# Optimization experiments

Measured on AMD Instinct MI355X. Metric: run time of the kernel, lower is better.

The kernel has to match this reference:

```python
import jax, jax.numpy as jnp
import numpy as np

NUM_CLASSES = 128
COST_CLS = 2.0
COST_BBOX = 0.25
ALPHA = 0.25
GAMMA = 2.0
BBOX_NORM = np.array([1.0, 1.0, 1.0, 0.1, 0.1, 0.1, 1.0, 1.0, 0.1, 0.1], dtype=np.float32)


def _lsa(cost):
    # Jonker-Volgenant style shortest augmenting path Hungarian (e-maxx formulation).
    # cost: (n, m) float64 with n <= m. Returns col4row: for each row i, assigned column.
    n, m = cost.shape
    INF = 1e18
    a = np.zeros((n + 1, m + 1))
    a[1:, 1:] = cost
    u = np.zeros(n + 1)
    v = np.zeros(m + 1)
    p = np.zeros(m + 1, dtype=np.int64)   # p[j]: row (1-indexed) assigned to col j
    way = np.zeros(m + 1, dtype=np.int64)
    cols = np.arange(1, m + 1)
    for i in range(1, n + 1):
        p[0] = i
        j0 = 0
        minv = np.full(m + 1, INF)
        used = np.zeros(m + 1, dtype=bool)
        while True:
            used[j0] = True
            i0 = p[j0]
            cur = a[i0, 1:] - u[i0] - v[1:]
            better = (~used[1:]) & (cur < minv[1:])
            jb = cols[better]
            minv[jb] = cur[better]
            way[jb] = j0
            free = cols[~used[1:]]
            j1 = free[np.argmin(minv[free])]
            delta = minv[j1]
            uj = np.flatnonzero(used)
            u[p[uj]] += delta
            v[uj] -= delta
            nj = np.flatnonzero(~used)
            minv[nj] -= delta
            j0 = int(j1)
            if p[j0] == 0:
                break
        while j0:
            j1 = way[j0]
            p[j0] = p[j1]
            j0 = j1
    col4row = np.zeros(n, dtype=np.int64)
    for j in range(1, m + 1):
        if p[j]:
            col4row[p[j] - 1] = j - 1
    return col4row


def _match(cls_scores, bbox_preds, gt_labels, gt_bboxes):
    # Matching is done under no_grad in the original; host-side numpy mirrors scipy lsa.
    cs = np.asarray(cls_scores, np.float64)
    bp = np.asarray(bbox_preds, np.float64)
    gl = np.asarray(gt_labels)
    gb = np.asarray(gt_bboxes, np.float64)
    B = cs.shape[0]
    norm = BBOX_NORM.astype(np.float64)
    pred_idx = np.zeros(gl.shape, dtype=np.int64)
    for b in range(B):
        prob = 1.0 / (1.0 + np.exp(-np.clip(cs[b], -20.0, 20.0)))
        cost_cls = -prob[:, gl[b]]                                   # (Q, G)
        pn = np.clip(bp[b] / norm, -100, 100)
        gn = np.clip(gb[b] / norm, -100, 100)
        cost_bbox = np.abs(pn[:, None, :] - gn[None, :, :]).sum(-1)  # (Q, G) L1 cdist
        C = COST_CLS * cost_cls + COST_BBOX * cost_bbox
        pred_idx[b] = _lsa(C.T)   # for each gt g, its matched query index
    return pred_idx


def setup_inputs() -> dict:
    key = jax.random.key(0)
    k1, k2, k3, k4 = jax.random.split(key, 4)
    B, Q, G, C = 64, 2048, 64, NUM_CLASSES
    return {
        "cls_scores": jax.random.normal(k1, (B, Q, C), jnp.float32),
        "bbox_preds": jax.random.normal(k2, (B, Q, 10), jnp.float32),
        "gt_labels": jax.random.randint(k3, (B, G), 0, C),
        "gt_bboxes": jax.random.normal(k4, (B, G, 10), jnp.float32),
    }


def reference(cls_scores, bbox_preds, gt_labels, gt_bboxes):
    pred_idx = jnp.asarray(_match(cls_scores, bbox_preds, gt_labels, gt_bboxes))  # [B, G]
    B, Q, C = cls_scores.shape
    G = gt_labels.shape[1]
    b_idx = jnp.arange(B)[:, None]
    # one-hot classification targets at matched (query, label) positions
    onehot = jnp.zeros((B, Q, C), cls_scores.dtype).at[b_idx, pred_idx, gt_labels].set(1.0)
    prob = jax.nn.sigmoid(cls_scores)
    ce = -(onehot * jax.nn.log_sigmoid(cls_scores)
           + (1.0 - onehot) * jax.nn.log_sigmoid(-cls_scores))
    p_t = prob * onehot + (1.0 - prob) * (1.0 - onehot)
    focal_w = (ALPHA * onehot + (1.0 - ALPHA) * (1.0 - onehot)) * (1.0 - p_t) ** GAMMA
    loss_cls = (ce * focal_w).sum() / (G * B)   # per-batch sum / num_gt, then mean over B
    norm = jnp.asarray(BBOX_NORM)
    mp = bbox_preds[b_idx, pred_idx]            # [B, G, 10] matched predictions
    mg = gt_bboxes                              # gt_indices == arange(G): every gt matched
    loss_bbox = jnp.abs(mp / norm - mg / norm).mean()
    ml = cls_scores[b_idx, pred_idx]
    pos_acc = (jnp.argmax(ml, -1) == gt_labels).astype(jnp.float32).mean()
    xyz_err = jnp.abs(mp[..., :3] - mg[..., :3]).mean()
    matched = jnp.float32(G)
    return jnp.stack([loss_cls, loss_bbox, matched, pos_acc, xyz_err])
```

## Files before the change

### kernel.cpp

```cpp
#include <hip/hip_runtime.h>
#include <hip/hip_fp16.h>
#include <math.h>

#define NB 64
#define NQ 2048
#define NG 64
#define NC 128
#define TPB 256

#define WS_NEG   0
#define WS_POS   16384
#define WS_PRED  147456
#define WS_COST  163840
#define WS_NEED  (163840 + (size_t)NB * NG * NQ * 2)

__device__ __forceinline__ float normd(int d) {
    return (d == 3 || d == 4 || d == 5 || d == 8 || d == 9) ? 0.1f : 1.0f;
}
__device__ __forceinline__ float softplus_f(float x) {
    return x > 0.f ? x + log1pf(expf(-x)) : log1pf(expf(x));
}
__device__ __forceinline__ double neg_term(float x) {
    float s = 1.f / (1.f + expf(-x));
    return (double)(0.75f * s * s * softplus_f(x));
}
__device__ __forceinline__ double pos_term(float x) {
    float s = 1.f / (1.f + expf(-x));
    float om = 1.f - s;
    return (double)(0.25f * om * om * softplus_f(-x));
}
__device__ __forceinline__ float neg_term_fast(float x) {
    const float m = fmaxf(x, 0.f);
    const float a = __expf(x - m);
    const float bq = __expf(-m);
    const float den = a + bq;
    const float s = __fdividef(a, den);
    const float sp = m + __logf(den);
    return 0.75f * s * s * sp;
}

__device__ __forceinline__ unsigned dpp_min6(unsigned key) {
    unsigned t;
    t = (unsigned)__builtin_amdgcn_update_dpp((int)key, (int)key, 0x111, 0xF, 0xF, false);
    key = t < key ? t : key;
    t = (unsigned)__builtin_amdgcn_update_dpp((int)key, (int)key, 0x112, 0xF, 0xF, false);
    key = t < key ? t : key;
    t = (unsigned)__builtin_amdgcn_update_dpp((int)key, (int)key, 0x114, 0xF, 0xF, false);
    key = t < key ? t : key;
    t = (unsigned)__builtin_amdgcn_update_dpp((int)key, (int)key, 0x118, 0xF, 0xF, false);
    key = t < key ? t : key;
    t = (unsigned)__builtin_amdgcn_update_dpp((int)key, (int)key, 0x142, 0xF, 0xF, false);
    key = t < key ? t : key;
    t = (unsigned)__builtin_amdgcn_update_dpp((int)key, (int)key, 0x143, 0xF, 0xF, false);
    key = t < key ? t : key;
    return key;
}

__global__ __launch_bounds__(TPB) void cost_neg_kernel(
    const float* __restrict__ cls, const float* __restrict__ bp,
    const int* __restrict__ gl, const float* __restrict__ gb,
    unsigned short* __restrict__ Ch, double* __restrict__ negP)
{
    const int b = blockIdx.x >> 5;
    const int q0 = (blockIdx.x & 31) << 6;
    const int tid = threadIdx.x;
    __shared__ float cls_s[64 * 129];
    __shared__ float pn_s[10 * 64];
    __shared__ float gn_s[64 * 10];
    __shared__ int lbl_s[64];

    double negsum = 0.0;
    const float* clsb = cls + ((size_t)b * NQ + q0) * NC;
    const float4* cls4 = reinterpret_cast<const float4*>(clsb);
    #pragma unroll
    for (int it = 0; it < 8; ++it) {
        const int idx4 = it * TPB + tid;
        const float4 xv = cls4[idx4];
        const int e0 = idx4 << 2;
        float* dst = &cls_s[(e0 >> 7) * 129 + (e0 & 127)];
        dst[0] = xv.x; dst[1] = xv.y; dst[2] = xv.z; dst[3] = xv.w;
        const float s4 = neg_term_fast(xv.x) + neg_term_fast(xv.y)
                       + neg_term_fast(xv.z) + neg_term_fast(xv.w);
        negsum += (double)s4;
    }
    const float* bpb = bp + ((size_t)b * NQ + q0) * 10;
    for (int idx = tid; idx < 640; idx += TPB) {
        const int q = idx / 10, d = idx % 10;
        const float val = bpb[idx] / normd(d);
        pn_s[d * 64 + q] = fminf(100.f, fmaxf(-100.f, val));
    }
    const float* gbb = gb + (size_t)b * NG * 10;
    for (int idx = tid; idx < 640; idx += TPB) {
        const int g = idx / 10, d = idx % 10;
        const float val = gbb[idx] / normd(d);
        gn_s[g * 10 + d] = fminf(100.f, fmaxf(-100.f, val));
    }
    if (tid < NG) lbl_s[tid] = gl[b * NG + tid];
    __syncthreads();

    const int q = tid & 63;
    float pnq[10];
    #pragma unroll
    for (int d = 0; d < 10; ++d) pnq[d] = pn_s[d * 64 + q];
    for (int g = tid >> 6; g < NG; g += 4) {
        const int lbl = lbl_s[g];
        float x = cls_s[q * 129 + lbl];
        x = fminf(20.f, fmaxf(-20.f, x));
        const float s = __fdividef(1.f, 1.f + __expf(-x));
        float cb = 0.f;
        #pragma unroll
        for (int d = 0; d < 10; ++d) cb += fabsf(pnq[d] - gn_s[g * 10 + d]);
        const float cost = -2.f * s + 0.25f * cb;
        Ch[((size_t)(b * NG + g)) * NQ + q0 + q] =
            __builtin_bit_cast(unsigned short, __float2half_rn(cost));
    }

    #pragma unroll
    for (int off = 32; off; off >>= 1) negsum += __shfl_down(negsum, off);
    __shared__ double bsum[4];
    if ((tid & 63) == 0) bsum[tid >> 6] = negsum;
    __syncthreads();
    if (tid == 0) negP[blockIdx.x] = bsum[0] + bsum[1] + bsum[2] + bsum[3];
}

__device__ __forceinline__ void jv_row(
    const int i, uint4 (&buf)[4], const unsigned short* __restrict__ Cb16,
    float (&vv)[32], unsigned& amask, const int lane, const int qbase,
    float* u, float* usedD, int* p, int* way32)
{
    float cf[32];
    #pragma unroll
    for (int m = 0; m < 4; ++m) {
        const unsigned arr[4] = {buf[m].x, buf[m].y, buf[m].z, buf[m].w};
        #pragma unroll
        for (int d = 0; d < 4; ++d) {
            const __half2 h = __builtin_bit_cast(__half2, arr[d]);
            cf[m * 8 + d * 2]     = __low2float(h);
            cf[m * 8 + d * 2 + 1] = __high2float(h);
        }
    }
    float madj[32];
    unsigned m0 = 0xFFFFFFFFu, m1 = 0xFFFFFFFFu, m2 = 0xFFFFFFFFu, m3 = 0xFFFFFFFFu;
    #pragma unroll
    for (int k = 0; k < 32; ++k) {
        const float cand = cf[k] - vv[k];
        madj[k] = cand;
        const unsigned kb = (__float_as_uint(cand) & 0xFFFFF800u) | (unsigned)(qbase + k);
        if ((k & 3) == 0)      m0 = kb < m0 ? kb : m0;
        else if ((k & 3) == 1) m1 = kb < m1 ? kb : m1;
        else if ((k & 3) == 2) m2 = kb < m2 ? kb : m2;
        else                   m3 = kb < m3 ? kb : m3;
    }
    if (i + 2 <= NG) {
        const uint4* rp = reinterpret_cast<const uint4*>(
                              Cb16 + (size_t)(i + 1) * NQ) + lane * 4;
        buf[0] = rp[0]; buf[1] = rp[1]; buf[2] = rp[2]; buf[3] = rp[3];
    }
    const unsigned ma = m0 < m1 ? m0 : m1;
    const unsigned mb = m2 < m3 ? m2 : m3;
    unsigned gkey = (unsigned)__builtin_amdgcn_readlane(
                        (int)dpp_min6(ma < mb ? ma : mb), 63);
    int q1 = (int)(gkey & 2047u);
    float D = __uint_as_float(gkey & 0xFFFFF800u);
    int ow = q1 >> 5, kk = q1 & 31;
    unsigned am_ow = (unsigned)__builtin_amdgcn_readlane((int)amask, ow);

    if (!((am_ow >> kk) & 1u)) {
        if (lane == 0) { u[i] += D; p[q1 + 1] = i; }
    } else {
        unsigned um = 0;
        if (lane == ow) { um |= 1u << kk; usedD[q1 + 1] = D; }
        #pragma unroll
        for (int k = 0; k < 32; ++k)
            if (k == kk && lane == ow) madj[k] = 1e30f;
        int j0 = q1 + 1;
        int i0 = p[j0];
        while (true) {
            const float s = u[i0] - D;
            const uint4* rp = reinterpret_cast<const uint4*>(
                                  Cb16 + (size_t)(i0 - 1) * NQ) + lane * 4;
            const uint4 t[4] = {rp[0], rp[1], rp[2], rp[3]};
            float tc[32];
            #pragma unroll
            for (int m = 0; m < 4; ++m) {
                const unsigned arr[4] = {t[m].x, t[m].y, t[m].z, t[m].w};
                #pragma unroll
                for (int d = 0; d < 4; ++d) {
                    const __half2 h = __builtin_bit_cast(__half2, arr[d]);
                    tc[m * 8 + d * 2]     = __low2float(h);
                    tc[m * 8 + d * 2 + 1] = __high2float(h);
                }
            }
            unsigned bk = 0xFFFFFFFFu;
            #pragma unroll
            for (int k = 0; k < 32; ++k) {
                const float cand = tc[k] - vv[k] - s;
                if (!((um >> k) & 1u) && cand < madj[k]) {
                    madj[k] = cand;
                    way32[qbase + k + 1] = (i << 16) | j0;
                }
                const unsigned kb = (__float_as_uint(madj[k]) & 0xFFFFF800u)
                                  | (unsigned)(qbase + k);
                bk = kb < bk ? kb : bk;
            }
            gkey = (unsigned)__builtin_amdgcn_readlane((int)dpp_min6(bk), 63);
            q1 = (int)(gkey & 2047u);
            D = __uint_as_float(gkey & 0xFFFFF800u);
            ow = q1 >> 5; kk = q1 & 31;
            am_ow = (unsigned)__builtin_amdgcn_readlane((int)amask, ow);
            if (!((am_ow >> kk) & 1u)) break;
            if (lane == ow) { um |= 1u << kk; usedD[q1 + 1] = D; }
            #pragma unroll
            for (int k = 0; k < 32; ++k)
                if (k == kk && lane == ow) madj[k] = 1e30f;
            j0 = q1 + 1;
            i0 = p[j0];
        }
        #pragma unroll
        for (int k = 0; k < 32; ++k) {
            if ((um >> k) & 1u) {
                const int j = qbase + k + 1;
                const float dd = D - usedD[j];
                vv[k] -= dd;
                u[p[j]] += dd;
            }
        }
        if (lane == 0) {
            u[i] += D;
            int j = q1 + 1;
            while (true) {
                const int w = way32[j];
                const int par = ((w >> 16) == i) ? (w & 0xFFFF) : 0;
                p[j] = par ? p[par] : i;
                if (!par) break;
                j = par;
            }
        }
    }
    if (lane == ow) amask |= 1u << kk;
}

__global__ __launch_bounds__(64, 1) void hungarian6_kernel(
    const unsigned short* __restrict__ Ch, int* __restrict__ pred)
{
    const int b = blockIdx.x;
    const int lane = threadIdx.x;
    __shared__ float u[NG + 1];
    __shared__ float usedD[NQ + 1];
    __shared__ int p[NQ + 1];
    __shared__ int way32[NQ + 1];

    for (int j = lane; j <= NQ; j += 64) { p[j] = 0; way32[j] = 0; }
    if (lane <= NG) u[lane] = 0.f;
    __syncthreads();

    const unsigned short* Cb16 = Ch + (size_t)b * NG * NQ;
    const int qbase = lane << 5;

    float vv[32];
    #pragma unroll
    for (int k = 0; k < 32; ++k) vv[k] = -16.f;
    unsigned amask = 0;

    uint4 A[4], B[4];
    {
        const uint4* r0 = reinterpret_cast<const uint4*>(Cb16) + lane * 4;
        const uint4* r1 = reinterpret_cast<const uint4*>(Cb16 + NQ) + lane * 4;
        A[0] = r0[0]; A[1] = r0[1]; A[2] = r0[2]; A[3] = r0[3];
        B[0] = r1[0]; B[1] = r1[1]; B[2] = r1[2]; B[3] = r1[3];
    }

    for (int i = 1; i <= NG; i += 2) {
        jv_row(i,     A, Cb16, vv, amask, lane, qbase, u, usedD, p, way32);
        jv_row(i + 1, B, Cb16, vv, amask, lane, qbase, u, usedD, p, way32);
    }

    for (int j = lane + 1; j <= NQ; j += 64) {
        const int pi = p[j];
        if (pi > 0) pred[b * NG + pi - 1] = j - 1;
    }
}

__global__ __launch_bounds__(TPB) void hungarian_fb_kernel(
    const float* __restrict__ cls, const float* __restrict__ bp,
    const int* __restrict__ gl, const float* __restrict__ gb,
    int* __restrict__ pred)
{
    const int b = blockIdx.x;
    const int tid = threadIdx.x;
    __shared__ float pn[10][NQ];
    __shared__ float gn[NG][10];
    __shared__ int lbls[NG];
    __shared__ double u[NG + 1];
    __shared__ double v[NQ + 1];
    __shared__ double minv[NQ + 1];
    __shared__ int p[NQ + 1];
    __shared__ int way[NQ + 1];
    __shared__ unsigned char used[NQ + 4];
    __shared__ double red_v[4];
    __shared__ int red_j[4];
    __shared__ int s_j0;
    __shared__ double s_delta;

    const float* bpb = bp + (size_t)b * NQ * 10;
    for (int idx = tid; idx < NQ * 10; idx += TPB) {
        int q = idx / 10, d = idx % 10;
        float val = bpb[idx] / normd(d);
        pn[d][q] = fminf(100.f, fmaxf(-100.f, val));
    }
    const float* gbb = gb + (size_t)b * NG * 10;
    for (int idx = tid; idx < NG * 10; idx += TPB) {
        int g = idx / 10, d = idx % 10;
        float val = gbb[idx] / normd(d);
        gn[g][d] = fminf(100.f, fmaxf(-100.f, val));
    }
    if (tid < NG) lbls[tid] = gl[b * NG + tid];
    for (int j = tid; j <= NQ; j += TPB) { v[j] = 0.0; p[j] = 0; way[j] = 0; }
    if (tid <= NG) u[tid] = 0.0;
    __syncthreads();

    const float* clsb = cls + (size_t)b * NQ * NC;

    for (int i = 1; i <= NG; ++i) {
        for (int j = tid; j <= NQ; j += TPB) { minv[j] = 1e18; used[j] = 0; }
        if (tid == 0) { p[0] = i; s_j0 = 0; }
        __syncthreads();
        while (true) {
            const int j0 = s_j0;
            if (tid == 0) used[j0] = 1;
            __syncthreads();
            const int i0 = p[j0];
            const int g = i0 - 1;
            const int lbl = lbls[g];
            const double ui0 = u[i0];
            double bestv = 1e30; int bestj = NQ + 1;
            for (int j = tid + 1; j <= NQ; j += TPB) {
                if (!used[j]) {
                    const int q = j - 1;
                    float x = clsb[(size_t)q * NC + lbl];
                    x = fminf(20.f, fmaxf(-20.f, x));
                    const double prob = 1.0 / (1.0 + exp((double)(-x)));
                    float cb = 0.f;
                    #pragma unroll
                    for (int d = 0; d < 10; ++d) cb += fabsf(pn[d][q] - gn[g][d]);
                    const double cur = -2.0 * prob + 0.25 * (double)cb - ui0 - v[j];
                    if (cur < minv[j]) { minv[j] = cur; way[j] = j0; }
                    const double mv = minv[j];
                    if (mv < bestv) { bestv = mv; bestj = j; }
                }
            }
            #pragma unroll
            for (int off = 32; off; off >>= 1) {
                const double ov = __shfl_down(bestv, off);
                const int oj = __shfl_down(bestj, off);
                if (ov < bestv || (ov == bestv && oj < bestj)) { bestv = ov; bestj = oj; }
            }
            if ((tid & 63) == 0) { red_v[tid >> 6] = bestv; red_j[tid >> 6] = bestj; }
            __syncthreads();
            if (tid == 0) {
                for (int w = 1; w < 4; ++w)
                    if (red_v[w] < bestv || (red_v[w] == bestv && red_j[w] < bestj)) {
                        bestv = red_v[w]; bestj = red_j[w];
                    }
                s_delta = bestv; s_j0 = bestj;
            }
            __syncthreads();
            const double delta = s_delta;
            const int j1 = s_j0;
            for (int j = tid; j <= NQ; j += TPB) {
                if (used[j]) { u[p[j]] += delta; v[j] -= delta; }
                else minv[j] -= delta;
            }
            __syncthreads();
            if (p[j1] == 0) break;
        }
        if (tid == 0) {
            int j = s_j0;
            while (j) { const int jn = way[j]; p[j] = p[jn]; j = jn; }
        }
        __syncthreads();
    }

    for (int j = tid + 1; j <= NQ; j += TPB) {
        const int pi = p[j];
        if (pi > 0) pred[b * NG + pi - 1] = j - 1;
    }
}

__global__ __launch_bounds__(TPB) void neg_fb_kernel(const float* __restrict__ cls,
                                                     double* __restrict__ negP, long n4) {
    const long stride = (long)gridDim.x * blockDim.x;
    double sum = 0.0;
    for (long i = (long)blockIdx.x * blockDim.x + threadIdx.x; i < n4; i += stride) {
        const float4 xv = reinterpret_cast<const float4*>(cls)[i];
        sum += (double)neg_term_fast(xv.x) + (double)neg_term_fast(xv.y)
             + (double)neg_term_fast(xv.z) + (double)neg_term_fast(xv.w);
    }
    #pragma unroll
    for (int off = 32; off; off >>= 1) sum += __shfl_down(sum, off);
    __shared__ double bsum[4];
    if ((threadIdx.x & 63) == 0) bsum[threadIdx.x >> 6] = sum;
    __syncthreads();
    if (threadIdx.x == 0) negP[blockIdx.x] = bsum[0] + bsum[1] + bsum[2] + bsum[3];
}

__global__ __launch_bounds__(TPB) void pos_kernel(
    const float* __restrict__ cls, const float* __restrict__ bp,
    const int* __restrict__ gl, const float* __restrict__ gb,
    const int* __restrict__ pred, double* __restrict__ posP)
{
    const int wid = (int)((blockIdx.x * blockDim.x + threadIdx.x) >> 6);
    const int lane = threadIdx.x & 63;
    if (wid >= NB * NG) return;
    const int b = wid >> 6;
    const int pq = pred[wid];
    const int lbl = gl[wid];
    const float* row = cls + ((size_t)b * NQ + pq) * NC;
    const float v1 = row[lane];
    const float v2 = row[lane + 64];
    float bv; int bi;
    if (v2 > v1) { bv = v2; bi = lane + 64; } else { bv = v1; bi = lane; }
    #pragma unroll
    for (int off = 32; off; off >>= 1) {
        const float ov = __shfl_down(bv, off);
        const int oi = __shfl_down(bi, off);
        if (ov > bv || (ov == bv && oi < bi)) { bv = ov; bi = oi; }
    }
    const float xl = __shfl(v1, lbl & 63);
    const float xh = __shfl(v2, lbl & 63);
    const float x = (lbl < 64) ? xl : xh;
    double bterm = 0.0, xterm = 0.0;
    if (lane < 10) {
        const float mp = bp[((size_t)b * NQ + pq) * 10 + lane];
        const float mg = gb[(size_t)wid * 10 + lane];
        const float nr = normd(lane);
        bterm = (double)fabsf(mp / nr - mg / nr);
        if (lane < 3) xterm = (double)fabsf(mp - mg);
    }
    #pragma unroll
    for (int off = 8; off; off >>= 1) {
        bterm += __shfl_down(bterm, off);
        xterm += __shfl_down(xterm, off);
    }
    if (lane == 0) {
        double* e = posP + (size_t)wid * 4;
        e[0] = pos_term(x) - neg_term(x);
        e[1] = bterm;
        e[2] = (bi == lbl) ? 1.0 : 0.0;
        e[3] = xterm;
    }
}

__global__ __launch_bounds__(TPB) void final_kernel(const double* __restrict__ ws,
                                                    float* __restrict__ out) {
    const int tid = threadIdx.x;
    const double* negP = ws;
    const double* posP = ws + 2048;
    double s[5] = {0, 0, 0, 0, 0};
    for (int i = tid; i < 2048; i += TPB) s[0] += negP[i];
    for (int i = tid; i < 4096; i += TPB) {
        const double* e = posP + (size_t)i * 4;
        s[1] += e[0]; s[2] += e[1]; s[3] += e[2]; s[4] += e[3];
    }
    __shared__ double red[4][5];
    #pragma unroll
    for (int c = 0; c < 5; ++c) {
        #pragma unroll
        for (int off = 32; off; off >>= 1) s[c] += __shfl_down(s[c], off);
    }
    if ((tid & 63) == 0) {
        #pragma unroll
        for (int c = 0; c < 5; ++c) red[tid >> 6][c] = s[c];
    }
    __syncthreads();
    if (tid == 0) {
        #pragma unroll
        for (int c = 0; c < 5; ++c) s[c] = red[0][c] + red[1][c] + red[2][c] + red[3][c];
        out[0] = (float)((s[0] + s[1]) / 4096.0);
        out[1] = (float)(s[2] / 40960.0);
        out[2] = 64.0f;
        out[3] = (float)(s[3] / 4096.0);
        out[4] = (float)(s[4] / 12288.0);
    }
}

extern "C" void kernel_launch(void* const* d_in, const int* in_sizes, int n_in,
                              void* d_out, int out_size, void* d_ws, size_t ws_size,
                              hipStream_t stream) {
    const float* cls = (const float*)d_in[0];
    const float* bp  = (const float*)d_in[1];
    const int*   gl  = (const int*)d_in[2];
    const float* gb  = (const float*)d_in[3];
    float* out = (float*)d_out;
    double* negP = (double*)((char*)d_ws + WS_NEG);
    double* posP = (double*)((char*)d_ws + WS_POS);
    int* pred    = (int*)((char*)d_ws + WS_PRED);
    unsigned short* Ch = (unsigned short*)((char*)d_ws + WS_COST);

    if (ws_size >= WS_NEED) {
        hipLaunchKernelGGL(cost_neg_kernel, dim3(NB * 32), dim3(TPB), 0, stream,
                           cls, bp, gl, gb, Ch, negP);
        hipLaunchKernelGGL(hungarian6_kernel, dim3(NB), dim3(64), 0, stream, Ch, pred);
    } else {
        hipLaunchKernelGGL(hungarian_fb_kernel, dim3(NB), dim3(TPB), 0, stream,
                           cls, bp, gl, gb, pred);
        const long n4 = (long)NB * NQ * NC / 4;
        hipLaunchKernelGGL(neg_fb_kernel, dim3(2048), dim3(TPB), 0, stream, cls, negP, n4);
    }
    hipLaunchKernelGGL(pos_kernel, dim3((NB * NG * 64) / TPB), dim3(TPB), 0, stream,
                       cls, bp, gl, gb, pred, posP);
    hipLaunchKernelGGL(final_kernel, dim3(1), dim3(TPB), 0, stream, (double*)d_ws, out);
}
```

Baseline: 189.3 us.

## Keep row duals in registers, deepen row prefetch, simplify focal term

The Hungarian kernel now holds the row dual u in a per-lane register instead of shared memory. It reads the value with readlane inside the augmenting search and applies dual updates through a small shared scratch array. Row prefetch goes from two buffered rows to four, and the first-pass min reduction is fused into the half-to-float conversion. The focal negative term uses a cheaper sigmoid/softplus form without the max-shift, which risks overflow for large positive logits, and the extra row buffers raise register pressure.

```diff
diff --git a/kernel.cpp b/kernel.cpp
--- a/kernel.cpp
+++ b/kernel.cpp
@@ -30,12 +30,10 @@
     return (double)(0.25f * om * om * softplus_f(-x));
 }
 __device__ __forceinline__ float neg_term_fast(float x) {
-    const float m = fmaxf(x, 0.f);
-    const float a = __expf(x - m);
-    const float bq = __expf(-m);
-    const float den = a + bq;
-    const float s = __fdividef(a, den);
-    const float sp = m + __logf(den);
+    const float t = __expf(x);
+    const float opt = 1.f + t;
+    const float s = t * __frcp_rn(opt);
+    const float sp = __logf(opt);
     return 0.75f * s * s * sp;
 }
 
@@ -55,6 +53,10 @@
     key = t < key ? t : key;
     return key;
 }
+__device__ __forceinline__ float readlane_f(float v, int lane) {
+    return __uint_as_float((unsigned)__builtin_amdgcn_readlane(
+               (int)__float_as_uint(v), lane));
+}
 
 __global__ __launch_bounds__(TPB) void cost_neg_kernel(
     const float* __restrict__ cls, const float* __restrict__ bp,
@@ -125,35 +127,30 @@
 
 __device__ __forceinline__ void jv_row(
     const int i, uint4 (&buf)[4], const unsigned short* __restrict__ Cb16,
-    float (&vv)[32], unsigned& amask, const int lane, const int qbase,
-    float* u, float* usedD, int* p, int* way32)
+    float (&vv)[32], unsigned& amask, float& u_reg, const int lane,
+    const int qbase, float* usedD, int* p, int* way32, float* uscr)
 {
-    float cf[32];
+    float madj[32];
+    unsigned m0 = 0xFFFFFFFFu, m1 = 0xFFFFFFFFu, m2 = 0xFFFFFFFFu, m3 = 0xFFFFFFFFu;
     #pragma unroll
     for (int m = 0; m < 4; ++m) {
         const unsigned arr[4] = {buf[m].x, buf[m].y, buf[m].z, buf[m].w};
         #pragma unroll
         for (int d = 0; d < 4; ++d) {
             const __half2 h = __builtin_bit_cast(__half2, arr[d]);
-            cf[m * 8 + d * 2]     = __low2float(h);
-            cf[m * 8 + d * 2 + 1] = __high2float(h);
+            const int k0 = m * 8 + d * 2;
+            const float c0 = __low2float(h) - vv[k0];
+            const float c1 = __high2float(h) - vv[k0 + 1];
+            madj[k0] = c0; madj[k0 + 1] = c1;
+            const unsigned kb0 = (__float_as_uint(c0) & 0xFFFFF800u) | (unsigned)(qbase + k0);
+            const unsigned kb1 = (__float_as_uint(c1) & 0xFFFFF800u) | (unsigned)(qbase + k0 + 1);
+            if (d & 1) { m2 = kb0 < m2 ? kb0 : m2;  m3 = kb1 < m3 ? kb1 : m3; }
+            else       { m0 = kb0 < m0 ? kb0 : m0;  m1 = kb1 < m1 ? kb1 : m1; }
         }
     }
-    float madj[32];
-    unsigned m0 = 0xFFFFFFFFu, m1 = 0xFFFFFFFFu, m2 = 0xFFFFFFFFu, m3 = 0xFFFFFFFFu;
-    #pragma unroll
-    for (int k = 0; k < 32; ++k) {
-        const float cand = cf[k] - vv[k];
-        madj[k] = cand;
-        const unsigned kb = (__float_as_uint(cand) & 0xFFFFF800u) | (unsigned)(qbase + k);
-        if ((k & 3) == 0)      m0 = kb < m0 ? kb : m0;
-        else if ((k & 3) == 1) m1 = kb < m1 ? kb : m1;
-        else if ((k & 3) == 2) m2 = kb < m2 ? kb : m2;
-        else                   m3 = kb < m3 ? kb : m3;
-    }
-    if (i + 2 <= NG) {
+    if (i + 4 <= NG) {
         const uint4* rp = reinterpret_cast<const uint4*>(
-                              Cb16 + (size_t)(i + 1) * NQ) + lane * 4;
+                              Cb16 + (size_t)(i + 3) * NQ) + lane * 4;
         buf[0] = rp[0]; buf[1] = rp[1]; buf[2] = rp[2]; buf[3] = rp[3];
     }
     const unsigned ma = m0 < m1 ? m0 : m1;
@@ -166,7 +163,8 @@
     unsigned am_ow = (unsigned)__builtin_amdgcn_readlane((int)amask, ow);
 
     if (!((am_ow >> kk) & 1u)) {
-        if (lane == 0) { u[i] += D; p[q1 + 1] = i; }
+        if (lane == i - 1) u_reg += D;
+        if (lane == 0) p[q1 + 1] = i;
     } else {
         unsigned um = 0;
         if (lane == ow) { um |= 1u << kk; usedD[q1 + 1] = D; }
@@ -176,7 +174,7 @@
         int j0 = q1 + 1;
         int i0 = p[j0];
         while (true) {
-            const float s = u[i0] - D;
+            const float s = readlane_f(u_reg, i0 - 1) - D;
             const uint4* rp = reinterpret_cast<const uint4*>(
                                   Cb16 + (size_t)(i0 - 1) * NQ) + lane * 4;
             const uint4 t[4] = {rp[0], rp[1], rp[2], rp[3]};
@@ -216,17 +214,19 @@
             j0 = q1 + 1;
             i0 = p[j0];
         }
+        uscr[lane] = 0.f;
         #pragma unroll
         for (int k = 0; k < 32; ++k) {
             if ((um >> k) & 1u) {
                 const int j = qbase + k + 1;
                 const float dd = D - usedD[j];
                 vv[k] -= dd;
-                u[p[j]] += dd;
+                uscr[p[j] - 1] = dd;
             }
         }
+        u_reg += uscr[lane];
+        if (lane == i - 1) u_reg += D;
         if (lane == 0) {
-            u[i] += D;
             int j = q1 + 1;
             while (true) {
                 const int w = way32[j];
@@ -240,18 +240,17 @@
     if (lane == ow) amask |= 1u << kk;
 }
 
-__global__ __launch_bounds__(64, 1) void hungarian6_kernel(
+__global__ __launch_bounds__(64, 1) void hungarian7_kernel(
     const unsigned short* __restrict__ Ch, int* __restrict__ pred)
 {
     const int b = blockIdx.x;
     const int lane = threadIdx.x;
-    __shared__ float u[NG + 1];
     __shared__ float usedD[NQ + 1];
     __shared__ int p[NQ + 1];
     __shared__ int way32[NQ + 1];
+    __shared__ float uscr[NG];
 
     for (int j = lane; j <= NQ; j += 64) { p[j] = 0; way32[j] = 0; }
-    if (lane <= NG) u[lane] = 0.f;
     __syncthreads();
 
     const unsigned short* Cb16 = Ch + (size_t)b * NG * NQ;
@@ -261,18 +260,25 @@
     #pragma unroll
     for (int k = 0; k < 32; ++k) vv[k] = -16.f;
     unsigned amask = 0;
-
-    uint4 A[4], B[4];
+    float u_reg = 0.f;
+
+    uint4 A[4], B[4], C4[4], D4[4];
     {
         const uint4* r0 = reinterpret_cast<const uint4*>(Cb16) + lane * 4;
         const uint4* r1 = reinterpret_cast<const uint4*>(Cb16 + NQ) + lane * 4;
-        A[0] = r0[0]; A[1] = r0[1]; A[2] = r0[2]; A[3] = r0[3];
-        B[0] = r1[0]; B[1] = r1[1]; B[2] = r1[2]; B[3] = r1[3];
-    }
-
-    for (int i = 1; i <= NG; i += 2) {
-        jv_row(i,     A, Cb16, vv, amask, lane, qbase, u, usedD, p, way32);
-        jv_row(i + 1, B, Cb16, vv, amask, lane, qbase, u, usedD, p, way32);
+        const uint4* r2 = reinterpret_cast<const uint4*>(Cb16 + 2 * NQ) + lane * 4;
+        const uint4* r3 = reinterpret_cast<const uint4*>(Cb16 + 3 * NQ) + lane * 4;
+        A[0] = r0[0];  A[1] = r0[1];  A[2] = r0[2];  A[3] = r0[3];
+        B[0] = r1[0];  B[1] = r1[1];  B[2] = r1[2];  B[3] = r1[3];
+        C4[0] = r2[0]; C4[1] = r2[1]; C4[2] = r2[2]; C4[3] = r2[3];
+        D4[0] = r3[0]; D4[1] = r3[1]; D4[2] = r3[2]; D4[3] = r3[3];
+    }
+
+    for (int i = 1; i <= NG; i += 4) {
+        jv_row(i,     A,  Cb16, vv, amask, u_reg, lane, qbase, usedD, p, way32, uscr);
+        jv_row(i + 1, B,  Cb16, vv, amask, u_reg, lane, qbase, usedD, p, way32, uscr);
+        jv_row(i + 2, C4, Cb16, vv, amask, u_reg, lane, qbase, usedD, p, way32, uscr);
+        jv_row(i + 3, D4, Cb16, vv, amask, u_reg, lane, qbase, usedD, p, way32, uscr);
     }
 
     for (int j = lane + 1; j <= NQ; j += 64) {
@@ -500,7 +506,7 @@
     if (ws_size >= WS_NEED) {
         hipLaunchKernelGGL(cost_neg_kernel, dim3(NB * 32), dim3(TPB), 0, stream,
                            cls, bp, gl, gb, Ch, negP);
-        hipLaunchKernelGGL(hungarian6_kernel, dim3(NB), dim3(64), 0, stream, Ch, pred);
+        hipLaunchKernelGGL(hungarian7_kernel, dim3(NB), dim3(64), 0, stream, Ch, pred);
     } else {
         hipLaunchKernelGGL(hungarian_fb_kernel, dim3(NB), dim3(TPB), 0, stream,
                            cls, bp, gl, gb, pred);
```

Result: faster. 184.1 us (-2.8%).
